# Performance work log

Measured on AMD Instinct MI355X. Metric: run time of the kernel, lower is better.

The kernel has to match this reference:

```python
import jax, jax.numpy as jnp
import numpy as np
import math

IN_F, OUT_F, NUM_TOKENS = 2048, 2048, 1024

def _make_tokens(num_tokens):
    positions = jnp.linspace(0.0, 1.0, num_tokens)[:, None]          # [T,1]
    freqs = jnp.linspace(1.0, 10.0, 32)[None, :]                     # [1,32]
    angles = positions * freqs * (2.0 * math.pi)                     # [T,32]
    return jnp.concatenate([jnp.sin(angles), jnp.cos(angles)], -1)   # [T,64]

def setup_inputs() -> dict:
    key = jax.random.key(0)
    k = jax.random.split(key, 5)
    x = jax.random.normal(k[0], (4, 4096, IN_F), dtype=jnp.float32)
    tokens = _make_tokens(NUM_TOKENS).astype(jnp.float32)            # [T,64]
    std = 0.02
    # weights stored as [in, out] so y = h @ W
    Wk1 = std * jax.random.normal(k[1], (64, 64), dtype=jnp.float32)
    Wk2 = std * jax.random.normal(k[2], (64, IN_F), dtype=jnp.float32)
    Wv1 = std * jax.random.normal(k[3], (64, 64), dtype=jnp.float32)
    Wv2 = std * jax.random.normal(k[4], (64, OUT_F), dtype=jnp.float32)
    return {"x": x, "tokens": tokens, "Wk1": Wk1, "Wk2": Wk2, "Wv1": Wv1, "Wv2": Wv2}

def reference(x, tokens, Wk1, Wk2, Wv1, Wv2):
    gelu = lambda h: jax.nn.gelu(h, approximate=False)  # torch F.gelu default is exact
    key_tokens = gelu(tokens @ Wk1) @ Wk2                # [T, in_features]
    value_tokens = gelu(tokens @ Wv1) @ Wv2              # [T, out_features]
    sim = jnp.einsum('bsd,td->bst', x, key_tokens)       # [B,S,T]
    T = sim.shape[-1]
    # row-wise scale: * sqrt(T) / sqrt(sum of squares over tokens)
    denom = jnp.sqrt(jnp.sum(sim * sim, axis=-1, keepdims=True))
    weights = gelu(sim * (jnp.sqrt(jnp.asarray(T, sim.dtype)) / denom))
    return jnp.einsum('bst,tf->bsf', weights, value_tokens)  # [B,S,out_features]
```

## Files before the change

kernel.cpp:

```cpp
#include <hip/hip_runtime.h>
#include <hip/hip_bf16.h>
#include <math.h>

typedef __attribute__((ext_vector_type(4))) float f32x4;
typedef __attribute__((ext_vector_type(8))) short bf16x8;
typedef __attribute__((ext_vector_type(4))) unsigned short u16x4;
typedef __attribute__((ext_vector_type(8))) unsigned short u16x8;
typedef __attribute__((ext_vector_type(2))) unsigned int u32x2;

__device__ __forceinline__ unsigned short f2b(float f) {
  unsigned int u = __builtin_bit_cast(unsigned int, f);
  u += 0x7fffu + ((u >> 16) & 1u);
  return (unsigned short)(u >> 16);
}
__device__ __forceinline__ float gelu_exact(float x) {
  return 0.5f * x * (1.0f + erff(x * 0.70710678118654752440f));
}

__global__ void prep(const float* __restrict__ tokens,
                     const float* __restrict__ Wk1, const float* __restrict__ Wv1,
                     const float* __restrict__ Wk2, const float* __restrict__ Wv2,
                     unsigned short* __restrict__ hkb, unsigned short* __restrict__ hvTb,
                     unsigned short* __restrict__ Wk2b, unsigned short* __restrict__ Wv2Tb) {
  const int tid = threadIdx.x;
  const int bx = blockIdx.x;
  if (bx < 256) {
    __shared__ float tok[4][64];
    const int tl = tid >> 6, j = tid & 63;
    const int t0 = bx * 4;
    tok[tl][j] = tokens[(size_t)(t0 + tl) * 64 + j];
    __syncthreads();
    float sk = 0.f, sv = 0.f;
    #pragma unroll 16
    for (int i = 0; i < 64; ++i) {
      float tv = tok[tl][i];
      sk += tv * Wk1[i * 64 + j];
      sv += tv * Wv1[i * 64 + j];
    }
    hkb[(size_t)(t0 + tl) * 64 + j]  = f2b(gelu_exact(sk));
    hvTb[(size_t)j * 1024 + t0 + tl] = f2b(gelu_exact(sv));
  } else if (bx < 272) {
    const int b = bx - 256;
    for (int i = 0; i < 8; ++i) {
      int idx = b * 2048 + i * 256 + tid;
      f32x4 v = ((const f32x4*)Wk2)[idx];
      u16x4 o; o[0] = f2b(v[0]); o[1] = f2b(v[1]); o[2] = f2b(v[2]); o[3] = f2b(v[3]);
      ((u16x4*)Wk2b)[idx] = o;
    }
  } else {
    __shared__ float t[64][65];
    const int f0 = (bx - 272) * 64;
    for (int i = 0; i < 16; ++i) {
      int idx = i * 256 + tid; int r = idx >> 6, c = idx & 63;
      t[r][c] = Wv2[(size_t)r * 2048 + f0 + c];
    }
    __syncthreads();
    for (int i = 0; i < 16; ++i) {
      int idx = i * 256 + tid; int r = idx >> 6, c = idx & 63;
      Wv2Tb[(size_t)(f0 + r) * 64 + c] = f2b(t[c][r]);
    }
  }
}

__global__ __launch_bounds__(256, 2)
void mainK(const float* __restrict__ x,
           const unsigned short* __restrict__ Wk2b,
           const unsigned short* __restrict__ hkb,
           const unsigned short* __restrict__ hvTb,
           const unsigned short* __restrict__ Wv2Tb,
           float* __restrict__ out) {
  __shared__ __align__(16) char smraw[76800];
  unsigned short* As = (unsigned short*)smraw;
  unsigned short* Bs = (unsigned short*)(smraw + 16384);
  float (*red)[4][64][4] = (float(*)[4][64][4])(smraw + 49152);
  unsigned short (*xw16)[72] = (unsigned short(*)[72])(smraw + 57344);
  unsigned short (*Pl)[32][152] = (unsigned short(*)[32][152])smraw;
  float (*redn)[2][16] = (float(*)[2][16])(smraw + 38912);
  float (*redw)[2][4][64][4] = (float(*)[2][4][64][4])(smraw + 39424);
  unsigned short* Ws = (unsigned short*)smraw;
  unsigned short* wvs = (unsigned short*)(smraw + 32768);
  float (*oS)[32][136] = (float(*)[32][136])(smraw + 36864);

  const int tid = threadIdx.x, wave = tid >> 6, lane = tid & 63;
  const int lrow = lane & 15, q = lane >> 4;
  const int r0 = blockIdx.x * 32;
  const int tw = wave * 256;

  {
    const int mt = wave & 1, h = wave >> 1;
    f32x4 aR[4]; u16x8 bR[4];
    f32x4 acc[4] = {};

#define P1_LOAD(sidx)                                                                     \
    do { _Pragma("unroll") for (int i = 0; i < 4; ++i) {                                  \
      int u4 = (wave * 4 + i) * 4 + (lane >> 4); int rr = u4 >> 1, ah = u4 & 1;           \
      aR[i] = *(const f32x4*)&x[(size_t)(r0 + rr) * 2048 + ah * 1024 + (sidx) * 64 + (lane & 15) * 4]; \
      int lin = (wave * 4 + i) * 8 + (lane >> 3); int t = lin >> 1, bh = lin & 1;         \
      bR[i] = *(const u16x8*)&Wk2b[(size_t)t * 2048 + bh * 1024 + (sidx) * 64 + (lane & 7) * 8]; \
    } } while (0)

#define P1_WRITE(buf)                                                                     \
    do { _Pragma("unroll") for (int i = 0; i < 4; ++i) {                                  \
      int u4 = (wave * 4 + i) * 4 + (lane >> 4); int rr = u4 >> 1, ah = u4 & 1;           \
      int uu = ((lane & 15) >> 1) ^ (rr & 7); u16x4 o;                                    \
      o[0] = f2b(aR[i][0]); o[1] = f2b(aR[i][1]); o[2] = f2b(aR[i][2]); o[3] = f2b(aR[i][3]); \
      *(u16x4*)&As[(buf) * 4096 + (rr * 2 + ah) * 64 + (uu << 3) + (lane & 1) * 4] = o;   \
      int lin = (wave * 4 + i) * 8 + (lane >> 3); int t = lin >> 1, bh = lin & 1;         \
      *(u16x8*)&Bs[(buf) * 8192 + (t * 2 + bh) * 64 + (((lane & 7) ^ (t & 7)) << 3)] = bR[i]; \
    } } while (0)

    P1_LOAD(0);
    P1_WRITE(0);
    P1_LOAD(1);
    __syncthreads();

    #pragma unroll 1
    for (int s = 0; s < 16; ++s) {
      const int cb = s & 1, nb = cb ^ 1;
      if (s + 1 < 16) P1_WRITE(nb);
      if (s + 2 < 16) P1_LOAD(s + 2);
      #pragma unroll
      for (int kk = 0; kk < 2; ++kk) {
        const int ar = mt * 16 + lrow;
        bf16x8 af = *(const bf16x8*)&As[cb * 4096 + (ar * 2 + h) * 64 + (((kk * 4 + q) ^ (ar & 7)) << 3)];
        #pragma unroll
        for (int nt = 0; nt < 4; ++nt) {
          const int br = nt * 16 + lrow;
          bf16x8 bf = *(const bf16x8*)&Bs[cb * 8192 + (br * 2 + h) * 64 + (((kk * 4 + q) ^ (br & 7)) << 3)];
          acc[nt] = __builtin_amdgcn_mfma_f32_16x16x32_bf16(af, bf, acc[nt], 0, 0, 0);
        }
      }
      __syncthreads();
    }
#undef P1_LOAD
#undef P1_WRITE

    if (h == 1) {
      #pragma unroll
      for (int nt = 0; nt < 4; ++nt) *(f32x4*)&red[mt][nt][lane][0] = acc[nt];
    }
    __syncthreads();
    if (h == 0) {
      #pragma unroll
      for (int nt = 0; nt < 4; ++nt) {
        f32x4 s2 = acc[nt] + *(const f32x4*)&red[mt][nt][lane][0];
        #pragma unroll
        for (int r = 0; r < 4; ++r)
          xw16[mt * 16 + q * 4 + r][nt * 16 + lrow] = f2b(s2[r]);
      }
    }
    __syncthreads();
  }

  {
    bf16x8 xb[2][2];
    #pragma unroll
    for (int mi = 0; mi < 2; ++mi)
      #pragma unroll
      for (int kk = 0; kk < 2; ++kk)
        xb[mi][kk] = *(const bf16x8*)&xw16[mi * 16 + lrow][kk * 32 + q * 8];

    f32x4 acc[16][2] = {};
    #pragma unroll
    for (int t16 = 0; t16 < 16; ++t16)
      #pragma unroll
      for (int kk = 0; kk < 2; ++kk) {
        bf16x8 a = *(const bf16x8*)&hkb[(size_t)(tw + t16 * 16 + lrow) * 64 + kk * 32 + q * 8];
        #pragma unroll
        for (int mi = 0; mi < 2; ++mi)
          acc[t16][mi] = __builtin_amdgcn_mfma_f32_16x16x32_bf16(a, xb[mi][kk], acc[t16][mi], 0, 0, 0);
      }

    float ss[2] = {0.f, 0.f};
    #pragma unroll
    for (int t16 = 0; t16 < 16; ++t16)
      #pragma unroll
      for (int mi = 0; mi < 2; ++mi)
        #pragma unroll
        for (int r = 0; r < 4; ++r)
          ss[mi] += acc[t16][mi][r] * acc[t16][mi][r];
    #pragma unroll
    for (int mi = 0; mi < 2; ++mi) {
      ss[mi] += __shfl_xor(ss[mi], 16, 64);
      ss[mi] += __shfl_xor(ss[mi], 32, 64);
    }
    if (q == 0) { redn[wave][0][lrow] = ss[0]; redn[wave][1][lrow] = ss[1]; }
    __syncthreads();
    float scale[2];
    #pragma unroll
    for (int mi = 0; mi < 2; ++mi) {
      float t = redn[0][mi][lrow] + redn[1][mi][lrow] + redn[2][mi][lrow] + redn[3][mi][lrow];
      scale[mi] = 32.0f * rsqrtf(fmaxf(t, 1e-20f));
    }

    f32x4 wva[2][4] = {};
    #pragma unroll
    for (int c = 0; c < 2; ++c) {
      #pragma unroll
      for (int t8 = 0; t8 < 8; ++t8) {
        const int t16 = c * 8 + t8;
        #pragma unroll
        for (int mi = 0; mi < 2; ++mi) {
          float g0 = gelu_exact(acc[t16][mi][0] * scale[mi]);
          float g1 = gelu_exact(acc[t16][mi][1] * scale[mi]);
          float g2 = gelu_exact(acc[t16][mi][2] * scale[mi]);
          float g3 = gelu_exact(acc[t16][mi][3] * scale[mi]);
          u32x2 pw;
          pw[0] = (unsigned)f2b(g0) | ((unsigned)f2b(g1) << 16);
          pw[1] = (unsigned)f2b(g2) | ((unsigned)f2b(g3) << 16);
          *(u32x2*)&Pl[wave][mi * 16 + lrow][t8 * 16 + q * 4] = pw;
        }
      }
      #pragma unroll
      for (int kc = 0; kc < 4; ++kc) {
        bf16x8 pa0 = *(const bf16x8*)&Pl[wave][lrow][kc * 32 + q * 8];
        bf16x8 pa1 = *(const bf16x8*)&Pl[wave][16 + lrow][kc * 32 + q * 8];
        #pragma unroll
        for (int nt = 0; nt < 4; ++nt) {
          bf16x8 b = *(const bf16x8*)&hvTb[(size_t)(nt * 16 + lrow) * 1024 +
                                           tw + c * 128 + kc * 32 + q * 8];
          wva[0][nt] = __builtin_amdgcn_mfma_f32_16x16x32_bf16(pa0, b, wva[0][nt], 0, 0, 0);
          wva[1][nt] = __builtin_amdgcn_mfma_f32_16x16x32_bf16(pa1, b, wva[1][nt], 0, 0, 0);
        }
      }
    }

    #pragma unroll
    for (int mi = 0; mi < 2; ++mi)
      #pragma unroll
      for (int nt = 0; nt < 4; ++nt)
        *(f32x4*)&redw[wave][mi][nt][lane][0] = wva[mi][nt];
    __syncthreads();
    #pragma unroll
    for (int mi = 0; mi < 2; ++mi) {
      f32x4 s = *(const f32x4*)&redw[0][mi][wave][lane][0];
      s += *(const f32x4*)&redw[1][mi][wave][lane][0];
      s += *(const f32x4*)&redw[2][mi][wave][lane][0];
      s += *(const f32x4*)&redw[3][mi][wave][lane][0];
      #pragma unroll
      for (int r = 0; r < 4; ++r) {
        int m = mi * 16 + q * 4 + r, j = wave * 16 + lrow;
        wvs[m * 64 + (((j >> 3) ^ (m & 7)) << 3) + (j & 7)] = f2b(s[r]);
      }
    }
    __syncthreads();
  }

  {
    u16x8 wR[4];

#define P3_LOAD(fcx)                                                                      \
    do { _Pragma("unroll") for (int i = 0; i < 4; ++i) {                                  \
      int lin = (wave * 4 + i) * 64 + lane; int frow = lin >> 3, u = lin & 7;             \
      wR[i] = *(const u16x8*)&Wv2Tb[(size_t)((fcx) * 128 + frow) * 64 + u * 8];           \
    } } while (0)
#define P3_WRITE(buf)                                                                     \
    do { _Pragma("unroll") for (int i = 0; i < 4; ++i) {                                  \
      int lin = (wave * 4 + i) * 64 + lane; int frow = lin >> 3, u = lin & 7;             \
      *(u16x8*)&Ws[(buf) * 8192 + frow * 64 + ((u ^ (frow & 7)) << 3)] = wR[i];           \
    } } while (0)

    P3_LOAD(0);
    P3_WRITE(0);
    P3_LOAD(1);

    bf16x8 bw[2][2];
    #pragma unroll
    for (int mt = 0; mt < 2; ++mt)
      #pragma unroll
      for (int kk = 0; kk < 2; ++kk) {
        int row = mt * 16 + lrow;
        bw[mt][kk] = *(const bf16x8*)&wvs[row * 64 + (((kk * 4 + q) ^ (row & 7)) << 3)];
      }
    __syncthreads();

    #pragma unroll 1
    for (int fc = 0; fc < 16; ++fc) {
      const int cb = fc & 1, nb = cb ^ 1, ob = fc & 1;
      if (fc + 1 < 16) P3_WRITE(nb);
      if (fc + 2 < 16) P3_LOAD(fc + 2);
      #pragma unroll
      for (int ftl = 0; ftl < 2; ++ftl) {
        const int ft = wave * 2 + ftl;
        f32x4 a2[2] = {};
        #pragma unroll
        for (int kk = 0; kk < 2; ++kk) {
          const int frow = ft * 16 + lrow;
          bf16x8 af = *(const bf16x8*)&Ws[cb * 8192 + frow * 64 + (((kk * 4 + q) ^ (frow & 7)) << 3)];
          #pragma unroll
          for (int mt = 0; mt < 2; ++mt)
            a2[mt] = __builtin_amdgcn_mfma_f32_16x16x32_bf16(af, bw[mt][kk], a2[mt], 0, 0, 0);
        }
        #pragma unroll
        for (int mt = 0; mt < 2; ++mt)
          *(f32x4*)&oS[ob][mt * 16 + lrow][ft * 16 + q * 4] = a2[mt];
      }
      __syncthreads();
      #pragma unroll
      for (int i = 0; i < 4; ++i) {
        int row = (wave * 4 + i) * 2 + (lane >> 5);
        int c = (lane & 31) * 4;
        f32x4 v = *(const f32x4*)&oS[ob][row][c];
        *(f32x4*)&out[(size_t)(r0 + row) * 2048 + fc * 128 + c] = v;
      }
    }
#undef P3_LOAD
#undef P3_WRITE
  }
}

extern "C" void kernel_launch(void* const* d_in, const int* in_sizes, int n_in,
                              void* d_out, int out_size, void* d_ws, size_t ws_size,
                              hipStream_t stream) {
  (void)in_sizes; (void)n_in; (void)out_size; (void)ws_size;
  const float* x      = (const float*)d_in[0];
  const float* tokens = (const float*)d_in[1];
  const float* Wk1    = (const float*)d_in[2];
  const float* Wk2    = (const float*)d_in[3];
  const float* Wv1    = (const float*)d_in[4];
  const float* Wv2    = (const float*)d_in[5];

  char* ws = (char*)d_ws;
  unsigned short* hkb   = (unsigned short*)(ws);
  unsigned short* hvTb  = (unsigned short*)(ws + 131072);
  unsigned short* Wk2b  = (unsigned short*)(ws + 262144);
  unsigned short* Wv2Tb = (unsigned short*)(ws + 524288);

  hipLaunchKernelGGL(prep, dim3(304), dim3(256), 0, stream,
                     tokens, Wk1, Wv1, Wk2, Wv2, hkb, hvTb, Wk2b, Wv2Tb);
  hipLaunchKernelGGL(mainK, dim3(512), dim3(256), 0, stream,
                     x, Wk2b, hkb, hvTb, Wv2Tb, (float*)d_out);
}
```

Measured before the change: 75.77 us.

## Shrink LDS footprint to fit three blocks per CU with register double-buffering

Cuts shared memory from 76.8KB to about 48KB by single-buffering the LDS tiles and keeping two stages of global prefetch in registers instead. Launch bounds are raised to allow three resident blocks per CU. The similarity tile is split into two halves, with the first half spilled to LDS as bf16 before GELU to lower register pressure. A lighter barrier macro waits only on LDS counters, so global loads can stay in flight across it. In exchange there are more barriers per stage and an extra bf16 rounding of the pre-GELU similarity values.

```diff
diff --git a/kernel.cpp b/kernel.cpp
--- a/kernel.cpp
+++ b/kernel.cpp
@@ -13,9 +13,19 @@
   u += 0x7fffu + ((u >> 16) & 1u);
   return (unsigned short)(u >> 16);
 }
+__device__ __forceinline__ float b2f(unsigned short u) {
+  unsigned int v = ((unsigned int)u) << 16;
+  return __builtin_bit_cast(float, v);
+}
 __device__ __forceinline__ float gelu_exact(float x) {
   return 0.5f * x * (1.0f + erff(x * 0.70710678118654752440f));
 }
+
+#define LBAR do {                                               \
+    asm volatile("s_waitcnt lgkmcnt(0)" ::: "memory");          \
+    __builtin_amdgcn_s_barrier();                               \
+    __builtin_amdgcn_sched_barrier(0);                          \
+  } while (0)
 
 __global__ void prep(const float* __restrict__ tokens,
                      const float* __restrict__ Wk1, const float* __restrict__ Wv1,
@@ -62,24 +72,22 @@
   }
 }
 
-__global__ __launch_bounds__(256, 2)
+__global__ __launch_bounds__(256, 3)
 void mainK(const float* __restrict__ x,
            const unsigned short* __restrict__ Wk2b,
            const unsigned short* __restrict__ hkb,
            const unsigned short* __restrict__ hvTb,
            const unsigned short* __restrict__ Wv2Tb,
            float* __restrict__ out) {
-  __shared__ __align__(16) char smraw[76800];
-  unsigned short* As = (unsigned short*)smraw;
-  unsigned short* Bs = (unsigned short*)(smraw + 16384);
-  float (*red)[4][64][4] = (float(*)[4][64][4])(smraw + 49152);
-  unsigned short (*xw16)[72] = (unsigned short(*)[72])(smraw + 57344);
-  unsigned short (*Pl)[32][152] = (unsigned short(*)[32][152])smraw;
-  float (*redn)[2][16] = (float(*)[2][16])(smraw + 38912);
-  float (*redw)[2][4][64][4] = (float(*)[2][4][64][4])(smraw + 39424);
-  unsigned short* Ws = (unsigned short*)smraw;
-  unsigned short* wvs = (unsigned short*)(smraw + 32768);
-  float (*oS)[32][136] = (float(*)[32][136])(smraw + 36864);
+  __shared__ __align__(16) char smraw[48128];
+  unsigned short (*xw16)[72] = (unsigned short(*)[72])smraw;
+  unsigned short* wvs = (unsigned short*)(smraw + 4608);
+  unsigned short* As  = (unsigned short*)(smraw + 8704);
+  unsigned short* Bs  = (unsigned short*)(smraw + 16896);
+  float (*red)[4][64][4] = (float(*)[4][64][4])(smraw + 8704);
+  float (*redn)[2][16] = (float(*)[2][16])(smraw + 47616);
+  unsigned short* Ws  = (unsigned short*)(smraw + 8704);
+  float (*oS)[132] = (float(*)[132])(smraw + 25088);
 
   const int tid = threadIdx.x, wave = tid >> 6, lane = tid & 63;
   const int lrow = lane & 15, q = lane >> 4;
@@ -88,71 +96,77 @@
 
   {
     const int mt = wave & 1, h = wave >> 1;
-    f32x4 aR[4]; u16x8 bR[4];
+    f32x4 aR0[4], aR1[4]; u16x8 bR0[4], bR1[4];
     f32x4 acc[4] = {};
 
-#define P1_LOAD(sidx)                                                                     \
+#define P1_LOAD(sidx, AR, BR)                                                             \
     do { _Pragma("unroll") for (int i = 0; i < 4; ++i) {                                  \
       int u4 = (wave * 4 + i) * 4 + (lane >> 4); int rr = u4 >> 1, ah = u4 & 1;           \
-      aR[i] = *(const f32x4*)&x[(size_t)(r0 + rr) * 2048 + ah * 1024 + (sidx) * 64 + (lane & 15) * 4]; \
+      AR[i] = *(const f32x4*)&x[(size_t)(r0 + rr) * 2048 + ah * 1024 + (sidx) * 64 + (lane & 15) * 4]; \
       int lin = (wave * 4 + i) * 8 + (lane >> 3); int t = lin >> 1, bh = lin & 1;         \
-      bR[i] = *(const u16x8*)&Wk2b[(size_t)t * 2048 + bh * 1024 + (sidx) * 64 + (lane & 7) * 8]; \
-    } } while (0)
-
-#define P1_WRITE(buf)                                                                     \
+      BR[i] = *(const u16x8*)&Wk2b[(size_t)t * 2048 + bh * 1024 + (sidx) * 64 + (lane & 7) * 8]; \
+    } } while (0)
+
+#define P1_WRITE(AR, BR)                                                                  \
     do { _Pragma("unroll") for (int i = 0; i < 4; ++i) {                                  \
       int u4 = (wave * 4 + i) * 4 + (lane >> 4); int rr = u4 >> 1, ah = u4 & 1;           \
       int uu = ((lane & 15) >> 1) ^ (rr & 7); u16x4 o;                                    \
-      o[0] = f2b(aR[i][0]); o[1] = f2b(aR[i][1]); o[2] = f2b(aR[i][2]); o[3] = f2b(aR[i][3]); \
-      *(u16x4*)&As[(buf) * 4096 + (rr * 2 + ah) * 64 + (uu << 3) + (lane & 1) * 4] = o;   \
+      o[0] = f2b(AR[i][0]); o[1] = f2b(AR[i][1]); o[2] = f2b(AR[i][2]); o[3] = f2b(AR[i][3]); \
+      *(u16x4*)&As[(rr * 2 + ah) * 64 + (uu << 3) + (lane & 1) * 4] = o;                  \
       int lin = (wave * 4 + i) * 8 + (lane >> 3); int t = lin >> 1, bh = lin & 1;         \
-      *(u16x8*)&Bs[(buf) * 8192 + (t * 2 + bh) * 64 + (((lane & 7) ^ (t & 7)) << 3)] = bR[i]; \
-    } } while (0)
-
-    P1_LOAD(0);
-    P1_WRITE(0);
-    P1_LOAD(1);
-    __syncthreads();
-
+      *(u16x8*)&Bs[(t * 2 + bh) * 64 + (((lane & 7) ^ (t & 7)) << 3)] = BR[i];            \
+    } } while (0)
+
+#define P1_COMP()                                                                         \
+    do { _Pragma("unroll") for (int kk = 0; kk < 2; ++kk) {                               \
+      const int ar = mt * 16 + lrow;                                                      \
+      bf16x8 af = *(const bf16x8*)&As[(ar * 2 + h) * 64 + (((kk * 4 + q) ^ (ar & 7)) << 3)]; \
+      _Pragma("unroll") for (int nt = 0; nt < 4; ++nt) {                                  \
+        const int br = nt * 16 + lrow;                                                    \
+        bf16x8 bf = *(const bf16x8*)&Bs[(br * 2 + h) * 64 + (((kk * 4 + q) ^ (br & 7)) << 3)]; \
+        acc[nt] = __builtin_amdgcn_mfma_f32_16x16x32_bf16(af, bf, acc[nt], 0, 0, 0);      \
+      } } } while (0)
+
+    P1_LOAD(0, aR0, bR0);
+    P1_LOAD(1, aR1, bR1);
     #pragma unroll 1
-    for (int s = 0; s < 16; ++s) {
-      const int cb = s & 1, nb = cb ^ 1;
-      if (s + 1 < 16) P1_WRITE(nb);
-      if (s + 2 < 16) P1_LOAD(s + 2);
-      #pragma unroll
-      for (int kk = 0; kk < 2; ++kk) {
-        const int ar = mt * 16 + lrow;
-        bf16x8 af = *(const bf16x8*)&As[cb * 4096 + (ar * 2 + h) * 64 + (((kk * 4 + q) ^ (ar & 7)) << 3)];
-        #pragma unroll
-        for (int nt = 0; nt < 4; ++nt) {
-          const int br = nt * 16 + lrow;
-          bf16x8 bf = *(const bf16x8*)&Bs[cb * 8192 + (br * 2 + h) * 64 + (((kk * 4 + q) ^ (br & 7)) << 3)];
-          acc[nt] = __builtin_amdgcn_mfma_f32_16x16x32_bf16(af, bf, acc[nt], 0, 0, 0);
-        }
-      }
-      __syncthreads();
+    for (int s2 = 0; s2 < 16; s2 += 2) {
+      P1_WRITE(aR0, bR0);
+      LBAR;
+      P1_COMP();
+      if (s2 + 2 < 16) P1_LOAD(s2 + 2, aR0, bR0);
+      LBAR;
+      P1_WRITE(aR1, bR1);
+      LBAR;
+      P1_COMP();
+      if (s2 + 3 < 16) P1_LOAD(s2 + 3, aR1, bR1);
+      LBAR;
     }
 #undef P1_LOAD
 #undef P1_WRITE
+#undef P1_COMP
 
     if (h == 1) {
       #pragma unroll
       for (int nt = 0; nt < 4; ++nt) *(f32x4*)&red[mt][nt][lane][0] = acc[nt];
     }
-    __syncthreads();
+    LBAR;
     if (h == 0) {
       #pragma unroll
       for (int nt = 0; nt < 4; ++nt) {
-        f32x4 s2 = acc[nt] + *(const f32x4*)&red[mt][nt][lane][0];
+        f32x4 s2v = acc[nt] + *(const f32x4*)&red[mt][nt][lane][0];
         #pragma unroll
         for (int r = 0; r < 4; ++r)
-          xw16[mt * 16 + q * 4 + r][nt * 16 + lrow] = f2b(s2[r]);
-      }
-    }
-    __syncthreads();
+          xw16[mt * 16 + q * 4 + r][nt * 16 + lrow] = f2b(s2v[r]);
+      }
+    }
+    LBAR;
   }
 
   {
+    char* reg_w = smraw + 8704 + wave * 9728;
+    unsigned short (*PlW)[152] = (unsigned short(*)[152])reg_w;
+
     bf16x8 xb[2][2];
     #pragma unroll
     for (int mi = 0; mi < 2; ++mi)
@@ -160,32 +174,55 @@
       for (int kk = 0; kk < 2; ++kk)
         xb[mi][kk] = *(const bf16x8*)&xw16[mi * 16 + lrow][kk * 32 + q * 8];
 
-    f32x4 acc[16][2] = {};
-    #pragma unroll
-    for (int t16 = 0; t16 < 16; ++t16)
+    float ss[2] = {0.f, 0.f};
+
+    {
+      f32x4 a0[8][2] = {};
+      #pragma unroll
+      for (int t8 = 0; t8 < 8; ++t8)
+        #pragma unroll
+        for (int kk = 0; kk < 2; ++kk) {
+          bf16x8 a = *(const bf16x8*)&hkb[(size_t)(tw + t8 * 16 + lrow) * 64 + kk * 32 + q * 8];
+          #pragma unroll
+          for (int mi = 0; mi < 2; ++mi)
+            a0[t8][mi] = __builtin_amdgcn_mfma_f32_16x16x32_bf16(a, xb[mi][kk], a0[t8][mi], 0, 0, 0);
+        }
+      #pragma unroll
+      for (int t8 = 0; t8 < 8; ++t8)
+        #pragma unroll
+        for (int mi = 0; mi < 2; ++mi) {
+          #pragma unroll
+          for (int r = 0; r < 4; ++r) ss[mi] += a0[t8][mi][r] * a0[t8][mi][r];
+          u32x2 pw;
+          pw[0] = (unsigned)f2b(a0[t8][mi][0]) | ((unsigned)f2b(a0[t8][mi][1]) << 16);
+          pw[1] = (unsigned)f2b(a0[t8][mi][2]) | ((unsigned)f2b(a0[t8][mi][3]) << 16);
+          *(u32x2*)&PlW[mi * 16 + lrow][t8 * 16 + q * 4] = pw;
+        }
+    }
+    f32x4 a1[8][2] = {};
+    #pragma unroll
+    for (int t8 = 0; t8 < 8; ++t8)
       #pragma unroll
       for (int kk = 0; kk < 2; ++kk) {
-        bf16x8 a = *(const bf16x8*)&hkb[(size_t)(tw + t16 * 16 + lrow) * 64 + kk * 32 + q * 8];
+        bf16x8 a = *(const bf16x8*)&hkb[(size_t)(tw + 128 + t8 * 16 + lrow) * 64 + kk * 32 + q * 8];
         #pragma unroll
         for (int mi = 0; mi < 2; ++mi)
-          acc[t16][mi] = __builtin_amdgcn_mfma_f32_16x16x32_bf16(a, xb[mi][kk], acc[t16][mi], 0, 0, 0);
-      }
-
-    float ss[2] = {0.f, 0.f};
-    #pragma unroll
-    for (int t16 = 0; t16 < 16; ++t16)
+          a1[t8][mi] = __builtin_amdgcn_mfma_f32_16x16x32_bf16(a, xb[mi][kk], a1[t8][mi], 0, 0, 0);
+      }
+    #pragma unroll
+    for (int t8 = 0; t8 < 8; ++t8)
       #pragma unroll
       for (int mi = 0; mi < 2; ++mi)
         #pragma unroll
-        for (int r = 0; r < 4; ++r)
-          ss[mi] += acc[t16][mi][r] * acc[t16][mi][r];
+        for (int r = 0; r < 4; ++r) ss[mi] += a1[t8][mi][r] * a1[t8][mi][r];
+
     #pragma unroll
     for (int mi = 0; mi < 2; ++mi) {
       ss[mi] += __shfl_xor(ss[mi], 16, 64);
       ss[mi] += __shfl_xor(ss[mi], 32, 64);
     }
     if (q == 0) { redn[wave][0][lrow] = ss[0]; redn[wave][1][lrow] = ss[1]; }
-    __syncthreads();
+    LBAR;
     float scale[2];
     #pragma unroll
     for (int mi = 0; mi < 2; ++mi) {
@@ -195,33 +232,46 @@
 
     f32x4 wva[2][4] = {};
     #pragma unroll
-    for (int c = 0; c < 2; ++c) {
-      #pragma unroll
-      for (int t8 = 0; t8 < 8; ++t8) {
-        const int t16 = c * 8 + t8;
-        #pragma unroll
-        for (int mi = 0; mi < 2; ++mi) {
-          float g0 = gelu_exact(acc[t16][mi][0] * scale[mi]);
-          float g1 = gelu_exact(acc[t16][mi][1] * scale[mi]);
-          float g2 = gelu_exact(acc[t16][mi][2] * scale[mi]);
-          float g3 = gelu_exact(acc[t16][mi][3] * scale[mi]);
-          u32x2 pw;
-          pw[0] = (unsigned)f2b(g0) | ((unsigned)f2b(g1) << 16);
-          pw[1] = (unsigned)f2b(g2) | ((unsigned)f2b(g3) << 16);
-          *(u32x2*)&Pl[wave][mi * 16 + lrow][t8 * 16 + q * 4] = pw;
-        }
-      }
-      #pragma unroll
-      for (int kc = 0; kc < 4; ++kc) {
-        bf16x8 pa0 = *(const bf16x8*)&Pl[wave][lrow][kc * 32 + q * 8];
-        bf16x8 pa1 = *(const bf16x8*)&Pl[wave][16 + lrow][kc * 32 + q * 8];
-        #pragma unroll
-        for (int nt = 0; nt < 4; ++nt) {
-          bf16x8 b = *(const bf16x8*)&hvTb[(size_t)(nt * 16 + lrow) * 1024 +
-                                           tw + c * 128 + kc * 32 + q * 8];
-          wva[0][nt] = __builtin_amdgcn_mfma_f32_16x16x32_bf16(pa0, b, wva[0][nt], 0, 0, 0);
-          wva[1][nt] = __builtin_amdgcn_mfma_f32_16x16x32_bf16(pa1, b, wva[1][nt], 0, 0, 0);
-        }
+    for (int kc = 0; kc < 4; ++kc) {
+      u16x8 r0v = *(const u16x8*)&PlW[lrow][kc * 32 + q * 8];
+      u16x8 r1v = *(const u16x8*)&PlW[16 + lrow][kc * 32 + q * 8];
+      u16x8 p0, p1;
+      #pragma unroll
+      for (int j = 0; j < 8; ++j) {
+        p0[j] = f2b(gelu_exact(b2f(r0v[j]) * scale[0]));
+        p1[j] = f2b(gelu_exact(b2f(r1v[j]) * scale[1]));
+      }
+      bf16x8 pa0 = __builtin_bit_cast(bf16x8, p0);
+      bf16x8 pa1 = __builtin_bit_cast(bf16x8, p1);
+      #pragma unroll
+      for (int nt = 0; nt < 4; ++nt) {
+        bf16x8 b = *(const bf16x8*)&hvTb[(size_t)(nt * 16 + lrow) * 1024 + tw + kc * 32 + q * 8];
+        wva[0][nt] = __builtin_amdgcn_mfma_f32_16x16x32_bf16(pa0, b, wva[0][nt], 0, 0, 0);
+        wva[1][nt] = __builtin_amdgcn_mfma_f32_16x16x32_bf16(pa1, b, wva[1][nt], 0, 0, 0);
+      }
+    }
+    #pragma unroll
+    for (int t8 = 0; t8 < 8; ++t8)
+      #pragma unroll
+      for (int mi = 0; mi < 2; ++mi) {
+        float g0 = gelu_exact(a1[t8][mi][0] * scale[mi]);
+        float g1 = gelu_exact(a1[t8][mi][1] * scale[mi]);
+        float g2 = gelu_exact(a1[t8][mi][2] * scale[mi]);
+        float g3 = gelu_exact(a1[t8][mi][3] * scale[mi]);
+        u32x2 pw;
+        pw[0] = (unsigned)f2b(g0) | ((unsigned)f2b(g1) << 16);
+        pw[1] = (unsigned)f2b(g2) | ((unsigned)f2b(g3) << 16);
+        *(u32x2*)&PlW[mi * 16 + lrow][t8 * 16 + q * 4] = pw;
+      }
+    #pragma unroll
+    for (int kc = 0; kc < 4; ++kc) {
+      bf16x8 pa0 = *(const bf16x8*)&PlW[lrow][kc * 32 + q * 8];
+      bf16x8 pa1 = *(const bf16x8*)&PlW[16 + lrow][kc * 32 + q * 8];
+      #pragma unroll
+      for (int nt = 0; nt < 4; ++nt) {
+        bf16x8 b = *(const bf16x8*)&hvTb[(size_t)(nt * 16 + lrow) * 1024 + tw + 128 + kc * 32 + q * 8];
+        wva[0][nt] = __builtin_amdgcn_mfma_f32_16x16x32_bf16(pa0, b, wva[0][nt], 0, 0, 0);
+        wva[1][nt] = __builtin_amdgcn_mfma_f32_16x16x32_bf16(pa1, b, wva[1][nt], 0, 0, 0);
       }
     }
 
@@ -229,40 +279,58 @@
     for (int mi = 0; mi < 2; ++mi)
       #pragma unroll
       for (int nt = 0; nt < 4; ++nt)
-        *(f32x4*)&redw[wave][mi][nt][lane][0] = wva[mi][nt];
-    __syncthreads();
+        *(f32x4*)(reg_w + (size_t)((mi * 4 + nt) * 64 + lane) * 16) = wva[mi][nt];
+    LBAR;
     #pragma unroll
     for (int mi = 0; mi < 2; ++mi) {
-      f32x4 s = *(const f32x4*)&redw[0][mi][wave][lane][0];
-      s += *(const f32x4*)&redw[1][mi][wave][lane][0];
-      s += *(const f32x4*)&redw[2][mi][wave][lane][0];
-      s += *(const f32x4*)&redw[3][mi][wave][lane][0];
+      f32x4 s = *(const f32x4*)(smraw + 8704 + 0 * 9728 + (size_t)((mi * 4 + wave) * 64 + lane) * 16);
+      s += *(const f32x4*)(smraw + 8704 + 1 * 9728 + (size_t)((mi * 4 + wave) * 64 + lane) * 16);
+      s += *(const f32x4*)(smraw + 8704 + 2 * 9728 + (size_t)((mi * 4 + wave) * 64 + lane) * 16);
+      s += *(const f32x4*)(smraw + 8704 + 3 * 9728 + (size_t)((mi * 4 + wave) * 64 + lane) * 16);
       #pragma unroll
       for (int r = 0; r < 4; ++r) {
         int m = mi * 16 + q * 4 + r, j = wave * 16 + lrow;
         wvs[m * 64 + (((j >> 3) ^ (m & 7)) << 3) + (j & 7)] = f2b(s[r]);
       }
     }
-    __syncthreads();
+    LBAR;
   }
 
   {
-    u16x8 wR[4];
-
-#define P3_LOAD(fcx)                                                                      \
+    u16x8 wR0[4], wR1[4];
+
+#define P3_LOAD(fcx, WR)                                                                  \
     do { _Pragma("unroll") for (int i = 0; i < 4; ++i) {                                  \
       int lin = (wave * 4 + i) * 64 + lane; int frow = lin >> 3, u = lin & 7;             \
-      wR[i] = *(const u16x8*)&Wv2Tb[(size_t)((fcx) * 128 + frow) * 64 + u * 8];           \
-    } } while (0)
-#define P3_WRITE(buf)                                                                     \
+      WR[i] = *(const u16x8*)&Wv2Tb[(size_t)((fcx) * 128 + frow) * 64 + u * 8];           \
+    } } while (0)
+#define P3_WRITE(WR)                                                                      \
     do { _Pragma("unroll") for (int i = 0; i < 4; ++i) {                                  \
       int lin = (wave * 4 + i) * 64 + lane; int frow = lin >> 3, u = lin & 7;             \
-      *(u16x8*)&Ws[(buf) * 8192 + frow * 64 + ((u ^ (frow & 7)) << 3)] = wR[i];           \
-    } } while (0)
-
-    P3_LOAD(0);
-    P3_WRITE(0);
-    P3_LOAD(1);
+      *(u16x8*)&Ws[frow * 64 + ((u ^ (frow & 7)) << 3)] = WR[i];                          \
+    } } while (0)
+#define P3_COMP()                                                                         \
+    do { _Pragma("unroll") for (int ftl = 0; ftl < 2; ++ftl) {                            \
+      const int ft = wave * 2 + ftl;                                                      \
+      f32x4 a2[2] = {};                                                                   \
+      _Pragma("unroll") for (int kk = 0; kk < 2; ++kk) {                                  \
+        const int frow = ft * 16 + lrow;                                                  \
+        bf16x8 af = *(const bf16x8*)&Ws[frow * 64 + (((kk * 4 + q) ^ (frow & 7)) << 3)];  \
+        _Pragma("unroll") for (int mt = 0; mt < 2; ++mt)                                  \
+          a2[mt] = __builtin_amdgcn_mfma_f32_16x16x32_bf16(af, bw[mt][kk], a2[mt], 0, 0, 0); \
+      }                                                                                   \
+      _Pragma("unroll") for (int mt = 0; mt < 2; ++mt)                                    \
+        *(f32x4*)&oS[mt * 16 + lrow][ft * 16 + q * 4] = a2[mt];                           \
+    } } while (0)
+#define P3_STORE(fcx)                                                                     \
+    do { _Pragma("unroll") for (int i = 0; i < 4; ++i) {                                  \
+      int row = (wave * 4 + i) * 2 + (lane >> 5); int c = (lane & 31) * 4;                \
+      f32x4 v = *(const f32x4*)&oS[row][c];                                               \
+      *(f32x4*)&out[(size_t)(r0 + row) * 2048 + (fcx) * 128 + c] = v;                     \
+    } } while (0)
+
+    P3_LOAD(0, wR0);
+    P3_LOAD(1, wR1);
 
     bf16x8 bw[2][2];
     #pragma unroll
@@ -272,40 +340,26 @@
         int row = mt * 16 + lrow;
         bw[mt][kk] = *(const bf16x8*)&wvs[row * 64 + (((kk * 4 + q) ^ (row & 7)) << 3)];
       }
-    __syncthreads();
 
     #pragma unroll 1
-    for (int fc = 0; fc < 16; ++fc) {
-      const int cb = fc & 1, nb = cb ^ 1, ob = fc & 1;
-      if (fc + 1 < 16) P3_WRITE(nb);
-      if (fc + 2 < 16) P3_LOAD(fc + 2);
-      #pragma unroll
-      for (int ftl = 0; ftl < 2; ++ftl) {
-        const int ft = wave * 2 + ftl;
-        f32x4 a2[2] = {};
-        #pragma unroll
-        for (int kk = 0; kk < 2; ++kk) {
-          const int frow = ft * 16 + lrow;
-          bf16x8 af = *(const bf16x8*)&Ws[cb * 8192 + frow * 64 + (((kk * 4 + q) ^ (frow & 7)) << 3)];
-          #pragma unroll
-          for (int mt = 0; mt < 2; ++mt)
-            a2[mt] = __builtin_amdgcn_mfma_f32_16x16x32_bf16(af, bw[mt][kk], a2[mt], 0, 0, 0);
-        }
-        #pragma unroll
-        for (int mt = 0; mt < 2; ++mt)
-          *(f32x4*)&oS[ob][mt * 16 + lrow][ft * 16 + q * 4] = a2[mt];
-      }
-      __syncthreads();
-      #pragma unroll
-      for (int i = 0; i < 4; ++i) {
-        int row = (wave * 4 + i) * 2 + (lane >> 5);
-        int c = (lane & 31) * 4;
-        f32x4 v = *(const f32x4*)&oS[ob][row][c];
-        *(f32x4*)&out[(size_t)(r0 + row) * 2048 + fc * 128 + c] = v;
-      }
+    for (int fc2 = 0; fc2 < 16; fc2 += 2) {
+      P3_WRITE(wR0);
+      LBAR;
+      P3_COMP();
+      if (fc2 + 2 < 16) P3_LOAD(fc2 + 2, wR0);
+      LBAR;
+      P3_STORE(fc2);
+      P3_WRITE(wR1);
+      LBAR;
+      P3_COMP();
+      if (fc2 + 3 < 16) P3_LOAD(fc2 + 3, wR1);
+      LBAR;
+      P3_STORE(fc2 + 1);
     }
 #undef P3_LOAD
 #undef P3_WRITE
+#undef P3_COMP
+#undef P3_STORE
   }
 }
 
```

After: 78.24 us. +3.3%, slower.
